# Kernel tuning notes

Hardware: AMD Instinct MI355X
Metric: run time of the kernel (lower is better)

## Reference

```python
import jax, jax.numpy as jnp
import numpy as np

N_NODES = 100000

def gcn_conv(x, W, b, src, dst):
    n = x.shape[0]
    loop = jnp.arange(n, dtype=src.dtype)
    src_f = jnp.concatenate([src, loop])
    dst_f = jnp.concatenate([dst, loop])
    deg = jax.ops.segment_sum(jnp.ones_like(src_f, dtype=x.dtype), dst_f, num_segments=n)
    dinv = jnp.where(deg > 0, deg ** -0.5, 0.0)
    norm = dinv[src_f] * dinv[dst_f]              # [E+N]
    h = x @ W                                      # [N, out]
    msg = h[src_f] * norm[:, None]                 # gather + scale
    out = jax.ops.segment_sum(msg, dst_f, num_segments=n)
    return out + b

def setup_inputs() -> dict:
    key = jax.random.key(0)
    k1, k2, k3, k4, k5 = jax.random.split(key, 5)
    d = 128
    x = jax.random.normal(k1, (N_NODES, d), dtype=jnp.float32)
    e = jax.random.randint(k2, (2, 3200000), 0, N_NODES, dtype=jnp.int64)
    # Glorot-style init as in PyG GCNConv
    W1 = jax.random.normal(k3, (d, 64), dtype=jnp.float32) * (1.0 / np.sqrt(d))
    b1 = jnp.zeros((64,), dtype=jnp.float32)
    W2 = jax.random.normal(k4, (64, 1), dtype=jnp.float32) * (1.0 / np.sqrt(64))
    b2 = jnp.zeros((1,), dtype=jnp.float32)
    return {"x": x, "e": e, "W1": W1, "b1": b1, "W2": W2, "b2": b2}

def reference(x, e, W1, b1, W2, b2):
    src, dst = e[0], e[1]
    h = jax.nn.relu(gcn_conv(x, W1, b1, src, dst))
    return gcn_conv(h, W2, b2, src, dst)
```

## Files before the change

### kernel.cpp

```cpp
#include <hip/hip_runtime.h>
#include <hip/hip_bf16.h>


typedef short s8_t __attribute__((ext_vector_type(8)));
typedef float f4_t __attribute__((ext_vector_type(4)));

__device__ __forceinline__ float bf2f(unsigned short u) {
    union { unsigned int u; float f; } c; c.u = ((unsigned int)u) << 16; return c.f;
}
__device__ __forceinline__ unsigned short f2bf(float f) {
    union { float f; unsigned int u; } c; c.f = f;
    unsigned int u = c.u;
    unsigned int r = (u + 0x7fffu + ((u >> 16) & 1u)) >> 16;
    return (unsigned short)r;
}
__device__ __forceinline__ float loadF(const void* p, int i, int isbf) {
    return isbf ? bf2f(((const unsigned short*)p)[i]) : ((const float*)p)[i];
}
__device__ __forceinline__ int edgeIdx(const void* e, long long i, int is64) {
    return is64 ? (int)((const long long*)e)[i] : ((const int*)e)[i];
}

__global__ void k_detect(const void* e, const void* x, int* flags) {
    int lane = threadIdx.x;
    unsigned int ew = ((const unsigned int*)e)[2 * lane + 1];
    unsigned long long nz = __ballot(ew != 0);
    unsigned int xw = ((const unsigned int*)x)[lane];
    unsigned int low = xw & 0xffffu;
    unsigned int e8 = (low >> 7) & 0xffu;
    bool plaus = (low == 0u) || (e8 >= 110u && e8 <= 135u);
    unsigned long long pl = __ballot(plaus);
    if (lane == 0) {
        flags[0] = (nz == 0ull) ? 1 : 0;
        flags[1] = (__popcll(pl) > 32) ? 1 : 0;
    }
}

__global__ void k_prep(const void* W1, unsigned short* __restrict__ wT,
                       const int* flags) {
    if (!flags[1]) return;
    int tid = threadIdx.x;
    const unsigned short* w = (const unsigned short*)W1;
    for (int idx = tid; idx < 128 * 64; idx += 256) {
        int k = idx >> 6, n = idx & 63;
        wT[n * 128 + k] = w[idx];
    }
}

__global__ void k_prep32(const void* W1, unsigned short* __restrict__ wTh,
                         unsigned short* __restrict__ wTl, const int* flags) {
    if (flags[1]) return;
    int tid = threadIdx.x;
    const float* w = (const float*)W1;
    for (int idx = tid; idx < 128 * 64; idx += 256) {
        int k = idx >> 6, n = idx & 63;
        float v = w[idx];
        unsigned short h = f2bf(v);
        wTh[n * 128 + k] = h;
        wTl[n * 128 + k] = f2bf(v - bf2f(h));
    }
}

__launch_bounds__(256)
__global__ void k_hist(const void* e, int* __restrict__ histT, const int* flags,
                       int E, int B, int HB) {
    __shared__ int hist[1024];
    int tid = threadIdx.x;
    int is64 = flags[0];
    for (int f = tid; f < B; f += 256) hist[f] = 0;
    __syncthreads();
    int base = blockIdx.x * 4096;
    #pragma unroll
    for (int k = 0; k < 16; ++k) {
        int i = base + k * 256 + tid;
        if (i < E) {
            int d = edgeIdx(e, (long long)E + i, is64);
            atomicAdd(&hist[d >> 9], 1);
        }
    }
    __syncthreads();
    for (int f = tid; f < B; f += 256)
        histT[(long long)f * HB + blockIdx.x] = hist[f];
}

__global__ void k_scanA(int* __restrict__ data, int* __restrict__ partial, int M) {
    __shared__ int s[256];
    int tid = threadIdx.x;
    int i = blockIdx.x * 256 + tid;
    int v = (i < M) ? data[i] : 0;
    s[tid] = v; __syncthreads();
    for (int off = 1; off < 256; off <<= 1) {
        int t = (tid >= off) ? s[tid - off] : 0;
        __syncthreads(); s[tid] += t; __syncthreads();
    }
    if (i < M) data[i] = s[tid] - v;
    if (tid == 255) partial[blockIdx.x] = s[255];
}

__global__ void k_scanB(int* __restrict__ partial, int nP) {
    __shared__ int s[1024];
    int tid = threadIdx.x;
    int C = (nP + 1023) >> 10;
    int base = tid * C;
    int v[8]; int tot = 0;
    for (int j = 0; j < C; ++j) { v[j] = (base + j < nP) ? partial[base + j] : 0; tot += v[j]; }
    s[tid] = tot; __syncthreads();
    for (int off = 1; off < 1024; off <<= 1) {
        int t = (tid >= off) ? s[tid - off] : 0;
        __syncthreads(); s[tid] += t; __syncthreads();
    }
    int run = s[tid] - tot;
    for (int j = 0; j < C; ++j) { if (base + j < nP) { int tmp = v[j]; partial[base + j] = run; run += tmp; } }
}

__global__ void k_scanC(int* __restrict__ data, const int* __restrict__ partial,
                        int* __restrict__ bucketStart, int M, int HB, int B, int E) {
    int f = blockIdx.x * 256 + threadIdx.x;
    if (f < M) {
        int val = data[f] + partial[f >> 8];
        data[f] = val;
        int q = f / HB;
        if (f - q * HB == 0) bucketStart[q] = val;
    }
    if (f == 0) bucketStart[B] = E;
}

__launch_bounds__(256)
__global__ void k_part(const void* e, const int* __restrict__ histT,
                       int* __restrict__ part, const int* flags,
                       int E, int B, int HB) {
    __shared__ int lcur[1024];
    int tid = threadIdx.x;
    int is64 = flags[0];
    for (int f = tid; f < B; f += 256)
        lcur[f] = histT[(long long)f * HB + blockIdx.x];
    __syncthreads();
    int base = blockIdx.x * 4096;
    #pragma unroll
    for (int k = 0; k < 16; ++k) {
        int i = base + k * 256 + tid;
        if (i < E) {
            int s = edgeIdx(e, i, is64);
            int d = edgeIdx(e, (long long)E + i, is64);
            int pos = atomicAdd(&lcur[d >> 9], 1);
            part[pos] = s | ((d & 511) << 17);
        }
    }
}

__launch_bounds__(512)
__global__ void k_sort2(const int* __restrict__ part, const int* __restrict__ bucketStart,
                        int* __restrict__ srcSorted, int* __restrict__ start,
                        float* __restrict__ dinv, int N, int B) {
    __shared__ int cnt[512];
    __shared__ int s[512];
    __shared__ int cur[512];
    int tid = threadIdx.x, b = blockIdx.x;
    cnt[tid] = 0;
    __syncthreads();
    int lo = bucketStart[b], hi = bucketStart[b + 1];
    for (int idx = lo + tid; idx < hi; idx += 512)
        atomicAdd(&cnt[(part[idx] >> 17) & 511], 1);
    __syncthreads();
    int v = cnt[tid];
    s[tid] = v; __syncthreads();
    for (int off = 1; off < 512; off <<= 1) {
        int t = (tid >= off) ? s[tid - off] : 0;
        __syncthreads(); s[tid] += t; __syncthreads();
    }
    int base_ = lo + s[tid] - v;
    cur[tid] = base_;
    int node = b * 512 + tid;
    if (node < N) {
        start[node] = base_;
        dinv[node] = rsqrtf((float)(v + 1));
    }
    if (b == 0 && tid == 0) start[N] = bucketStart[B];
    __syncthreads();
    for (int idx = lo + tid; idx < hi; idx += 512) {
        int pw = part[idx];
        int pos = atomicAdd(&cur[(pw >> 17) & 511], 1);
        srcSorted[pos] = pw & 0x1FFFF;
    }
}

__launch_bounds__(256)
__global__ void k_gemm_bf(const void* x, const unsigned short* __restrict__ wT,
                          const float* __restrict__ dinv,
                          unsigned short* __restrict__ hb, const int* flags, int N) {
    if (!flags[1]) return;
    int tid = threadIdx.x;
    int lane = tid & 63, wv = tid >> 6;
    int q = lane >> 4, r = lane & 15;
    const unsigned short* xb = (const unsigned short*)x;
    int gw = blockIdx.x * 4 + wv;
    int nW = gridDim.x * 4;
    int RB = (N + 15) >> 4;
    for (int rb = gw; rb < RB; rb += nW) {
        int row0 = rb * 16;
        int arow = row0 + r;
        s8_t a[4];
        #pragma unroll
        for (int kk = 0; kk < 4; ++kk)
            a[kk] = (arow < N)
                ? *(const s8_t*)&xb[(long long)arow * 128 + kk * 32 + q * 8]
                : (s8_t)(short)0;
        f4_t acc[4];
        #pragma unroll
        for (int nt = 0; nt < 4; ++nt) acc[nt] = (f4_t){0.f, 0.f, 0.f, 0.f};
        #pragma unroll
        for (int nt = 0; nt < 4; ++nt) {
            #pragma unroll
            for (int kk = 0; kk < 4; ++kk) {
                s8_t b = *(const s8_t*)&wT[(nt * 16 + r) * 128 + kk * 32 + q * 8];
                acc[nt] = __builtin_amdgcn_mfma_f32_16x16x32_bf16(a[kk], b, acc[nt], 0, 0, 0);
            }
        }
        #pragma unroll
        for (int reg = 0; reg < 4; ++reg) {
            int row = row0 + q * 4 + reg;
            if (row < N) {
                float dv = dinv[row];
                #pragma unroll
                for (int nt = 0; nt < 4; ++nt)
                    hb[(long long)row * 64 + nt * 16 + r] = f2bf(acc[nt][reg] * dv);
            }
        }
    }
}

__launch_bounds__(256)
__global__ void k_gemm_x32(const void* x, const unsigned short* __restrict__ wTh,
                           const unsigned short* __restrict__ wTl,
                           const float* __restrict__ dinv,
                           unsigned short* __restrict__ hb, const int* flags, int N) {
    if (flags[1]) return;
    int tid = threadIdx.x;
    int lane = tid & 63, wv = tid >> 6;
    int q = lane >> 4, r = lane & 15;
    const float* xf = (const float*)x;
    int gw = blockIdx.x * 4 + wv;
    int nW = gridDim.x * 4;
    int RB = (N + 15) >> 4;
    for (int rb = gw; rb < RB; rb += nW) {
        int row0 = rb * 16;
        int arow = row0 + r;
        s8_t ah[4], al[4];
        #pragma unroll
        for (int kk = 0; kk < 4; ++kk) {
            f4_t x0 = (f4_t){0.f, 0.f, 0.f, 0.f}, x1 = x0;
            if (arow < N) {
                const float* p = &xf[(long long)arow * 128 + kk * 32 + q * 8];
                x0 = *(const f4_t*)p;
                x1 = *(const f4_t*)(p + 4);
            }
            #pragma unroll
            for (int j = 0; j < 4; ++j) {
                unsigned short h0 = f2bf(x0[j]);
                ah[kk][j] = (short)h0;
                al[kk][j] = (short)f2bf(x0[j] - bf2f(h0));
                unsigned short h1 = f2bf(x1[j]);
                ah[kk][4 + j] = (short)h1;
                al[kk][4 + j] = (short)f2bf(x1[j] - bf2f(h1));
            }
        }
        f4_t acc[4];
        #pragma unroll
        for (int nt = 0; nt < 4; ++nt) acc[nt] = (f4_t){0.f, 0.f, 0.f, 0.f};
        #pragma unroll
        for (int nt = 0; nt < 4; ++nt) {
            #pragma unroll
            for (int kk = 0; kk < 4; ++kk) {
                s8_t bh = *(const s8_t*)&wTh[(nt * 16 + r) * 128 + kk * 32 + q * 8];
                s8_t bl = *(const s8_t*)&wTl[(nt * 16 + r) * 128 + kk * 32 + q * 8];
                acc[nt] = __builtin_amdgcn_mfma_f32_16x16x32_bf16(ah[kk], bh, acc[nt], 0, 0, 0);
                acc[nt] = __builtin_amdgcn_mfma_f32_16x16x32_bf16(al[kk], bh, acc[nt], 0, 0, 0);
                acc[nt] = __builtin_amdgcn_mfma_f32_16x16x32_bf16(ah[kk], bl, acc[nt], 0, 0, 0);
            }
        }
        #pragma unroll
        for (int reg = 0; reg < 4; ++reg) {
            int row = row0 + q * 4 + reg;
            if (row < N) {
                float dv = dinv[row];
                #pragma unroll
                for (int nt = 0; nt < 4; ++nt)
                    hb[(long long)row * 64 + nt * 16 + r] = f2bf(acc[nt][reg] * dv);
            }
        }
    }
}

__launch_bounds__(256)
__global__ void k_agg1(const unsigned short* __restrict__ hb,
                       const float* __restrict__ dinv,
                       const int* __restrict__ start,
                       const int* __restrict__ srcSorted,
                       const void* b1, const void* W2, float* __restrict__ sbuf2,
                       const int* flags, int N) {
    int lane = threadIdx.x & 63;
    int node = (blockIdx.x * blockDim.x + threadIdx.x) >> 6;
    if (node >= N) return;
    int isbf = flags[1];
    float di = dinv[node];
    int base = start[node], cnt = start[node + 1] - base;
    float acc = bf2f(hb[(long long)node * 64 + lane]);
    for (int c = 0; c < cnt; c += 64) {
        int t = c + lane;
        int sidx = (t < cnt) ? srcSorted[base + t] : 0;
        int m = cnt - c; if (m > 64) m = 64;
        int t2 = 0;
        for (; t2 + 16 <= m; t2 += 16) {
            int s0  = __shfl(sidx, t2 + 0),  s1  = __shfl(sidx, t2 + 1);
            int s2  = __shfl(sidx, t2 + 2),  s3  = __shfl(sidx, t2 + 3);
            int s4  = __shfl(sidx, t2 + 4),  s5  = __shfl(sidx, t2 + 5);
            int s6  = __shfl(sidx, t2 + 6),  s7  = __shfl(sidx, t2 + 7);
            int s8  = __shfl(sidx, t2 + 8),  s9  = __shfl(sidx, t2 + 9);
            int s10 = __shfl(sidx, t2 + 10), s11 = __shfl(sidx, t2 + 11);
            int s12 = __shfl(sidx, t2 + 12), s13 = __shfl(sidx, t2 + 13);
            int s14 = __shfl(sidx, t2 + 14), s15 = __shfl(sidx, t2 + 15);
            unsigned short v0  = hb[(long long)s0  * 64 + lane];
            unsigned short v1  = hb[(long long)s1  * 64 + lane];
            unsigned short v2  = hb[(long long)s2  * 64 + lane];
            unsigned short v3  = hb[(long long)s3  * 64 + lane];
            unsigned short v4  = hb[(long long)s4  * 64 + lane];
            unsigned short v5  = hb[(long long)s5  * 64 + lane];
            unsigned short v6  = hb[(long long)s6  * 64 + lane];
            unsigned short v7  = hb[(long long)s7  * 64 + lane];
            unsigned short v8  = hb[(long long)s8  * 64 + lane];
            unsigned short v9  = hb[(long long)s9  * 64 + lane];
            unsigned short v10 = hb[(long long)s10 * 64 + lane];
            unsigned short v11 = hb[(long long)s11 * 64 + lane];
            unsigned short v12 = hb[(long long)s12 * 64 + lane];
            unsigned short v13 = hb[(long long)s13 * 64 + lane];
            unsigned short v14 = hb[(long long)s14 * 64 + lane];
            unsigned short v15 = hb[(long long)s15 * 64 + lane];
            acc += bf2f(v0);  acc += bf2f(v1);  acc += bf2f(v2);  acc += bf2f(v3);
            acc += bf2f(v4);  acc += bf2f(v5);  acc += bf2f(v6);  acc += bf2f(v7);
            acc += bf2f(v8);  acc += bf2f(v9);  acc += bf2f(v10); acc += bf2f(v11);
            acc += bf2f(v12); acc += bf2f(v13); acc += bf2f(v14); acc += bf2f(v15);
        }
        for (; t2 + 8 <= m; t2 += 8) {
            int s0 = __shfl(sidx, t2 + 0), s1 = __shfl(sidx, t2 + 1);
            int s2 = __shfl(sidx, t2 + 2), s3 = __shfl(sidx, t2 + 3);
            int s4 = __shfl(sidx, t2 + 4), s5 = __shfl(sidx, t2 + 5);
            int s6 = __shfl(sidx, t2 + 6), s7 = __shfl(sidx, t2 + 7);
            unsigned short v0 = hb[(long long)s0 * 64 + lane];
            unsigned short v1 = hb[(long long)s1 * 64 + lane];
            unsigned short v2 = hb[(long long)s2 * 64 + lane];
            unsigned short v3 = hb[(long long)s3 * 64 + lane];
            unsigned short v4 = hb[(long long)s4 * 64 + lane];
            unsigned short v5 = hb[(long long)s5 * 64 + lane];
            unsigned short v6 = hb[(long long)s6 * 64 + lane];
            unsigned short v7 = hb[(long long)s7 * 64 + lane];
            acc += bf2f(v0); acc += bf2f(v1); acc += bf2f(v2); acc += bf2f(v3);
            acc += bf2f(v4); acc += bf2f(v5); acc += bf2f(v6); acc += bf2f(v7);
        }
        for (; t2 < m; ++t2) {
            int s0 = __shfl(sidx, t2);
            acc += bf2f(hb[(long long)s0 * 64 + lane]);
        }
    }
    float v = acc * di + loadF(b1, lane, isbf);
    v = fmaxf(v, 0.f);
    float p = v * loadF(W2, lane, isbf);
    #pragma unroll
    for (int o = 32; o >= 1; o >>= 1) p += __shfl_xor(p, o);
    if (lane == 0) sbuf2[node] = p * di;
}

__launch_bounds__(256)
__global__ void k_agg2(const float* __restrict__ sbuf2, const float* __restrict__ dinv,
                       const int* __restrict__ start,
                       const int* __restrict__ srcSorted,
                       const void* b2, void* out, const int* flags, int N) {
    int lane = threadIdx.x & 63;
    int node = (blockIdx.x * blockDim.x + threadIdx.x) >> 6;
    if (node >= N) return;
    int isbf = flags[1];
    float di = dinv[node];
    int base = start[node], cnt = start[node + 1] - base;
    float part = 0.f;
    for (int t = lane; t < cnt; t += 64) part += sbuf2[srcSorted[base + t]];
    #pragma unroll
    for (int o = 32; o >= 1; o >>= 1) part += __shfl_xor(part, o);
    if (lane == 0) {
        float o_ = (part + sbuf2[node]) * di + loadF(b2, 0, isbf);
        if (isbf) ((unsigned short*)out)[node] = f2bf(o_);
        else      ((float*)out)[node] = o_;
    }
}

extern "C" void kernel_launch(void* const* d_in, const int* in_sizes, int n_in,
                              void* d_out, int out_size, void* d_ws, size_t ws_size,
                              hipStream_t stream) {
    const void* x  = d_in[0];
    const void* e  = d_in[1];
    const void* W1 = d_in[2];
    const void* b1 = d_in[3];
    const void* W2 = d_in[4];
    const void* b2 = d_in[5];
    int N = in_sizes[0] / 128;
    int E = in_sizes[1] / 2;
    int B  = (N + 511) / 512;
    int HB = (E + 4095) / 4096;
    int M  = B * HB;
    int nP = (M + 255) / 256;
    int NB = B * 512;
    int EP = ((E + 255) / 256) * 256;
    int RB = (N + 15) / 16;
    int GG = (RB + 3) / 4;

    int*   wsI         = (int*)d_ws;
    int*   flags       = wsI;
    unsigned short* wT  = (unsigned short*)(wsI + 256);
    unsigned short* wTh = (unsigned short*)(wsI + 256 + 4096);
    unsigned short* wTl = (unsigned short*)(wsI + 256 + 8192);
    int*   histT       = wsI + 256 + 12288;
    int*   partial     = histT + ((M + 255) / 256) * 256;
    int*   bucketStart = partial + ((nP + 255) / 256) * 256;
    float* dinv        = (float*)(bucketStart + 1040);
    float* sbuf2       = dinv + NB;
    int*   start       = (int*)(sbuf2 + NB);
    int*   srcSorted   = start + NB + 256;
    int*   part        = srcSorted + EP;
    unsigned short* hb = (unsigned short*)part;

    hipLaunchKernelGGL(k_detect, dim3(1), dim3(64), 0, stream, e, x, flags);
    hipLaunchKernelGGL(k_prep, dim3(1), dim3(256), 0, stream, W1, wT, flags);
    hipLaunchKernelGGL(k_prep32, dim3(1), dim3(256), 0, stream, W1, wTh, wTl, flags);
    hipLaunchKernelGGL(k_hist, dim3(HB), dim3(256), 0, stream, e, histT, flags, E, B, HB);
    hipLaunchKernelGGL(k_scanA, dim3(nP), dim3(256), 0, stream, histT, partial, M);
    hipLaunchKernelGGL(k_scanB, dim3(1), dim3(1024), 0, stream, partial, nP);
    hipLaunchKernelGGL(k_scanC, dim3(nP), dim3(256), 0, stream,
                       histT, partial, bucketStart, M, HB, B, E);
    hipLaunchKernelGGL(k_part, dim3(HB), dim3(256), 0, stream, e, histT, part, flags, E, B, HB);
    hipLaunchKernelGGL(k_sort2, dim3(B), dim3(512), 0, stream,
                       part, bucketStart, srcSorted, start, dinv, N, B);
    hipLaunchKernelGGL(k_gemm_bf, dim3(GG), dim3(256), 0, stream,
                       x, wT, dinv, hb, flags, N);
    hipLaunchKernelGGL(k_gemm_x32, dim3(GG), dim3(256), 0, stream,
                       x, wTh, wTl, dinv, hb, flags, N);
    hipLaunchKernelGGL(k_agg1, dim3((N + 3) / 4), dim3(256), 0, stream,
                       hb, dinv, start, srcSorted, b1, W2, sbuf2, flags, N);
    hipLaunchKernelGGL(k_agg2, dim3((N + 3) / 4), dim3(256), 0, stream,
                       sbuf2, dinv, start, srcSorted, b2, d_out, flags, N);
}
```

Before: 332.0 us.

## Split hidden features into quarter tables and aggregate 16 nodes per wave

The GEMM output is stored as four column-quarter tables of 16 bf16 features each, instead of one 64-wide row-major table. The first aggregation now has each wave handle 16 nodes and sweep the four quarter tables, with each 16-lane group gathering a different edge. The intent is to shrink the working set per gather pass so each quarter table fits better in cache, and to make gathered accesses 32-byte segments. It also merges the two prep kernels and the two GEMM kernels into single launches, and replaces round-to-nearest with truncation when splitting fp32 into hi/lo bf16. The cost is reading the edge lists four times and more complex control flow, and truncation slightly changes rounding.

```diff
diff --git a/kernel.cpp b/kernel.cpp
--- a/kernel.cpp
+++ b/kernel.cpp
@@ -4,6 +4,8 @@
 
 typedef short s8_t __attribute__((ext_vector_type(8)));
 typedef float f4_t __attribute__((ext_vector_type(4)));
+
+#define NPW 16
 
 __device__ __forceinline__ float bf2f(unsigned short u) {
     union { unsigned int u; float f; } c; c.u = ((unsigned int)u) << 16; return c.f;
@@ -36,28 +38,25 @@
     }
 }
 
-__global__ void k_prep(const void* W1, unsigned short* __restrict__ wT,
-                       const int* flags) {
-    if (!flags[1]) return;
-    int tid = threadIdx.x;
-    const unsigned short* w = (const unsigned short*)W1;
-    for (int idx = tid; idx < 128 * 64; idx += 256) {
-        int k = idx >> 6, n = idx & 63;
-        wT[n * 128 + k] = w[idx];
-    }
-}
-
-__global__ void k_prep32(const void* W1, unsigned short* __restrict__ wTh,
-                         unsigned short* __restrict__ wTl, const int* flags) {
-    if (flags[1]) return;
-    int tid = threadIdx.x;
-    const float* w = (const float*)W1;
-    for (int idx = tid; idx < 128 * 64; idx += 256) {
-        int k = idx >> 6, n = idx & 63;
-        float v = w[idx];
-        unsigned short h = f2bf(v);
-        wTh[n * 128 + k] = h;
-        wTl[n * 128 + k] = f2bf(v - bf2f(h));
+__global__ void k_prep_all(const void* W1, unsigned short* __restrict__ wT,
+                           unsigned short* __restrict__ wTh,
+                           unsigned short* __restrict__ wTl, const int* flags) {
+    int tid = threadIdx.x;
+    if (flags[1]) {
+        const unsigned short* w = (const unsigned short*)W1;
+        for (int idx = tid; idx < 128 * 64; idx += 256) {
+            int k = idx >> 6, n = idx & 63;
+            wT[n * 128 + k] = w[idx];
+        }
+    } else {
+        const float* w = (const float*)W1;
+        for (int idx = tid; idx < 128 * 64; idx += 256) {
+            int k = idx >> 6, n = idx & 63;
+            float v = w[idx];
+            unsigned short h = f2bf(v);
+            wTh[n * 128 + k] = h;
+            wTl[n * 128 + k] = f2bf(v - bf2f(h));
+        }
     }
 }
 
@@ -185,35 +184,76 @@
 }
 
 __launch_bounds__(256)
-__global__ void k_gemm_bf(const void* x, const unsigned short* __restrict__ wT,
-                          const float* __restrict__ dinv,
-                          unsigned short* __restrict__ hb, const int* flags, int N) {
-    if (!flags[1]) return;
+__global__ void k_gemm(const void* x, const unsigned short* __restrict__ wT,
+                       const unsigned short* __restrict__ wTh,
+                       const unsigned short* __restrict__ wTl,
+                       const float* __restrict__ dinv,
+                       unsigned short* __restrict__ hbq, const int* flags, int N) {
     int tid = threadIdx.x;
     int lane = tid & 63, wv = tid >> 6;
     int q = lane >> 4, r = lane & 15;
-    const unsigned short* xb = (const unsigned short*)x;
     int gw = blockIdx.x * 4 + wv;
     int nW = gridDim.x * 4;
     int RB = (N + 15) >> 4;
+    int isbf = flags[1];
     for (int rb = gw; rb < RB; rb += nW) {
         int row0 = rb * 16;
         int arow = row0 + r;
-        s8_t a[4];
-        #pragma unroll
-        for (int kk = 0; kk < 4; ++kk)
-            a[kk] = (arow < N)
-                ? *(const s8_t*)&xb[(long long)arow * 128 + kk * 32 + q * 8]
-                : (s8_t)(short)0;
         f4_t acc[4];
         #pragma unroll
         for (int nt = 0; nt < 4; ++nt) acc[nt] = (f4_t){0.f, 0.f, 0.f, 0.f};
-        #pragma unroll
-        for (int nt = 0; nt < 4; ++nt) {
+        if (isbf) {
+            const unsigned short* xb = (const unsigned short*)x;
+            s8_t a[4];
+            #pragma unroll
+            for (int kk = 0; kk < 4; ++kk)
+                a[kk] = (arow < N)
+                    ? *(const s8_t*)&xb[(long long)arow * 128 + kk * 32 + q * 8]
+                    : (s8_t)(short)0;
+            #pragma unroll
+            for (int nt = 0; nt < 4; ++nt) {
+                #pragma unroll
+                for (int kk = 0; kk < 4; ++kk) {
+                    s8_t b = *(const s8_t*)&wT[(nt * 16 + r) * 128 + kk * 32 + q * 8];
+                    acc[nt] = __builtin_amdgcn_mfma_f32_16x16x32_bf16(a[kk], b, acc[nt], 0, 0, 0);
+                }
+            }
+        } else {
+            const float* xf = (const float*)x;
+            s8_t ah[4], al[4];
             #pragma unroll
             for (int kk = 0; kk < 4; ++kk) {
-                s8_t b = *(const s8_t*)&wT[(nt * 16 + r) * 128 + kk * 32 + q * 8];
-                acc[nt] = __builtin_amdgcn_mfma_f32_16x16x32_bf16(a[kk], b, acc[nt], 0, 0, 0);
+                f4_t x0 = (f4_t){0.f, 0.f, 0.f, 0.f}, x1 = x0;
+                if (arow < N) {
+                    const float* p = &xf[(long long)arow * 128 + kk * 32 + q * 8];
+                    x0 = *(const f4_t*)p;
+                    x1 = *(const f4_t*)(p + 4);
+                }
+                #pragma unroll
+                for (int j = 0; j < 4; ++j) {
+                    union { float f; unsigned int u; } c0, h0, r0, c1, h1, r1;
+                    c0.f = x0[j];
+                    h0.u = c0.u & 0xffff0000u;
+                    ah[kk][j] = (short)(c0.u >> 16);
+                    r0.f = x0[j] - h0.f;
+                    al[kk][j] = (short)(r0.u >> 16);
+                    c1.f = x1[j];
+                    h1.u = c1.u & 0xffff0000u;
+                    ah[kk][4 + j] = (short)(c1.u >> 16);
+                    r1.f = x1[j] - h1.f;
+                    al[kk][4 + j] = (short)(r1.u >> 16);
+                }
+            }
+            #pragma unroll
+            for (int nt = 0; nt < 4; ++nt) {
+                #pragma unroll
+                for (int kk = 0; kk < 4; ++kk) {
+                    s8_t bh = *(const s8_t*)&wTh[(nt * 16 + r) * 128 + kk * 32 + q * 8];
+                    s8_t bl = *(const s8_t*)&wTl[(nt * 16 + r) * 128 + kk * 32 + q * 8];
+                    acc[nt] = __builtin_amdgcn_mfma_f32_16x16x32_bf16(ah[kk], bh, acc[nt], 0, 0, 0);
+                    acc[nt] = __builtin_amdgcn_mfma_f32_16x16x32_bf16(al[kk], bh, acc[nt], 0, 0, 0);
+                    acc[nt] = __builtin_amdgcn_mfma_f32_16x16x32_bf16(ah[kk], bl, acc[nt], 0, 0, 0);
+                }
             }
         }
         #pragma unroll
@@ -223,150 +263,82 @@
                 float dv = dinv[row];
                 #pragma unroll
                 for (int nt = 0; nt < 4; ++nt)
-                    hb[(long long)row * 64 + nt * 16 + r] = f2bf(acc[nt][reg] * dv);
+                    hbq[((long long)nt * N + row) * 16 + r] = f2bf(acc[nt][reg] * dv);
             }
         }
     }
 }
 
 __launch_bounds__(256)
-__global__ void k_gemm_x32(const void* x, const unsigned short* __restrict__ wTh,
-                           const unsigned short* __restrict__ wTl,
-                           const float* __restrict__ dinv,
-                           unsigned short* __restrict__ hb, const int* flags, int N) {
-    if (flags[1]) return;
-    int tid = threadIdx.x;
-    int lane = tid & 63, wv = tid >> 6;
-    int q = lane >> 4, r = lane & 15;
-    const float* xf = (const float*)x;
-    int gw = blockIdx.x * 4 + wv;
-    int nW = gridDim.x * 4;
-    int RB = (N + 15) >> 4;
-    for (int rb = gw; rb < RB; rb += nW) {
-        int row0 = rb * 16;
-        int arow = row0 + r;
-        s8_t ah[4], al[4];
-        #pragma unroll
-        for (int kk = 0; kk < 4; ++kk) {
-            f4_t x0 = (f4_t){0.f, 0.f, 0.f, 0.f}, x1 = x0;
-            if (arow < N) {
-                const float* p = &xf[(long long)arow * 128 + kk * 32 + q * 8];
-                x0 = *(const f4_t*)p;
-                x1 = *(const f4_t*)(p + 4);
-            }
-            #pragma unroll
-            for (int j = 0; j < 4; ++j) {
-                unsigned short h0 = f2bf(x0[j]);
-                ah[kk][j] = (short)h0;
-                al[kk][j] = (short)f2bf(x0[j] - bf2f(h0));
-                unsigned short h1 = f2bf(x1[j]);
-                ah[kk][4 + j] = (short)h1;
-                al[kk][4 + j] = (short)f2bf(x1[j] - bf2f(h1));
-            }
-        }
-        f4_t acc[4];
-        #pragma unroll
-        for (int nt = 0; nt < 4; ++nt) acc[nt] = (f4_t){0.f, 0.f, 0.f, 0.f};
-        #pragma unroll
-        for (int nt = 0; nt < 4; ++nt) {
-            #pragma unroll
-            for (int kk = 0; kk < 4; ++kk) {
-                s8_t bh = *(const s8_t*)&wTh[(nt * 16 + r) * 128 + kk * 32 + q * 8];
-                s8_t bl = *(const s8_t*)&wTl[(nt * 16 + r) * 128 + kk * 32 + q * 8];
-                acc[nt] = __builtin_amdgcn_mfma_f32_16x16x32_bf16(ah[kk], bh, acc[nt], 0, 0, 0);
-                acc[nt] = __builtin_amdgcn_mfma_f32_16x16x32_bf16(al[kk], bh, acc[nt], 0, 0, 0);
-                acc[nt] = __builtin_amdgcn_mfma_f32_16x16x32_bf16(ah[kk], bl, acc[nt], 0, 0, 0);
-            }
-        }
-        #pragma unroll
-        for (int reg = 0; reg < 4; ++reg) {
-            int row = row0 + q * 4 + reg;
-            if (row < N) {
-                float dv = dinv[row];
-                #pragma unroll
-                for (int nt = 0; nt < 4; ++nt)
-                    hb[(long long)row * 64 + nt * 16 + r] = f2bf(acc[nt][reg] * dv);
-            }
-        }
-    }
-}
-
-__launch_bounds__(256)
-__global__ void k_agg1(const unsigned short* __restrict__ hb,
+__global__ void k_agg1(const unsigned short* __restrict__ hbq,
                        const float* __restrict__ dinv,
                        const int* __restrict__ start,
                        const int* __restrict__ srcSorted,
                        const void* b1, const void* W2, float* __restrict__ sbuf2,
                        const int* flags, int N) {
     int lane = threadIdx.x & 63;
-    int node = (blockIdx.x * blockDim.x + threadIdx.x) >> 6;
-    if (node >= N) return;
+    int wid = (blockIdx.x * blockDim.x + threadIdx.x) >> 6;
+    int g = lane >> 4, r = lane & 15;
+    int n0 = wid * NPW;
+    if (n0 >= N) return;
+    float acc[NPW];
+    #pragma unroll
+    for (int i = 0; i < NPW; ++i) acc[i] = 0.f;
+    for (int q = 0; q < 4; ++q) {
+        const unsigned short* tab = hbq + (long long)q * N * 16;
+        #pragma unroll
+        for (int i = 0; i < NPW; ++i) {
+            int node = n0 + i;
+            if (node < N) {
+                int base = start[node];
+                int cnt  = start[node + 1] - base;
+                float a = 0.f;
+                for (int c = 0; c < cnt; c += 64) {
+                    int t = c + lane;
+                    int sidx = (t < cnt) ? srcSorted[base + t] : 0;
+                    int m = cnt - c; if (m > 64) m = 64;
+                    int t2 = 0;
+                    for (; t2 + 16 <= m; t2 += 16) {
+                        int e0 = __shfl(sidx, t2 + g);
+                        int e1 = __shfl(sidx, t2 + 4 + g);
+                        int e2 = __shfl(sidx, t2 + 8 + g);
+                        int e3 = __shfl(sidx, t2 + 12 + g);
+                        unsigned short v0 = tab[e0 * 16 + r];
+                        unsigned short v1 = tab[e1 * 16 + r];
+                        unsigned short v2 = tab[e2 * 16 + r];
+                        unsigned short v3 = tab[e3 * 16 + r];
+                        a += bf2f(v0); a += bf2f(v1);
+                        a += bf2f(v2); a += bf2f(v3);
+                    }
+                    for (; t2 < m; t2 += 4) {
+                        int e0 = __shfl(sidx, t2 + g);
+                        unsigned short v0 = tab[e0 * 16 + r];
+                        a += (t2 + g < m) ? bf2f(v0) : 0.f;
+                    }
+                }
+                a += __shfl_xor(a, 16);
+                a += __shfl_xor(a, 32);
+                acc[i] = (g == q) ? a : acc[i];
+            }
+        }
+    }
     int isbf = flags[1];
-    float di = dinv[node];
-    int base = start[node], cnt = start[node + 1] - base;
-    float acc = bf2f(hb[(long long)node * 64 + lane]);
-    for (int c = 0; c < cnt; c += 64) {
-        int t = c + lane;
-        int sidx = (t < cnt) ? srcSorted[base + t] : 0;
-        int m = cnt - c; if (m > 64) m = 64;
-        int t2 = 0;
-        for (; t2 + 16 <= m; t2 += 16) {
-            int s0  = __shfl(sidx, t2 + 0),  s1  = __shfl(sidx, t2 + 1);
-            int s2  = __shfl(sidx, t2 + 2),  s3  = __shfl(sidx, t2 + 3);
-            int s4  = __shfl(sidx, t2 + 4),  s5  = __shfl(sidx, t2 + 5);
-            int s6  = __shfl(sidx, t2 + 6),  s7  = __shfl(sidx, t2 + 7);
-            int s8  = __shfl(sidx, t2 + 8),  s9  = __shfl(sidx, t2 + 9);
-            int s10 = __shfl(sidx, t2 + 10), s11 = __shfl(sidx, t2 + 11);
-            int s12 = __shfl(sidx, t2 + 12), s13 = __shfl(sidx, t2 + 13);
-            int s14 = __shfl(sidx, t2 + 14), s15 = __shfl(sidx, t2 + 15);
-            unsigned short v0  = hb[(long long)s0  * 64 + lane];
-            unsigned short v1  = hb[(long long)s1  * 64 + lane];
-            unsigned short v2  = hb[(long long)s2  * 64 + lane];
-            unsigned short v3  = hb[(long long)s3  * 64 + lane];
-            unsigned short v4  = hb[(long long)s4  * 64 + lane];
-            unsigned short v5  = hb[(long long)s5  * 64 + lane];
-            unsigned short v6  = hb[(long long)s6  * 64 + lane];
-            unsigned short v7  = hb[(long long)s7  * 64 + lane];
-            unsigned short v8  = hb[(long long)s8  * 64 + lane];
-            unsigned short v9  = hb[(long long)s9  * 64 + lane];
-            unsigned short v10 = hb[(long long)s10 * 64 + lane];
-            unsigned short v11 = hb[(long long)s11 * 64 + lane];
-            unsigned short v12 = hb[(long long)s12 * 64 + lane];
-            unsigned short v13 = hb[(long long)s13 * 64 + lane];
-            unsigned short v14 = hb[(long long)s14 * 64 + lane];
-            unsigned short v15 = hb[(long long)s15 * 64 + lane];
-            acc += bf2f(v0);  acc += bf2f(v1);  acc += bf2f(v2);  acc += bf2f(v3);
-            acc += bf2f(v4);  acc += bf2f(v5);  acc += bf2f(v6);  acc += bf2f(v7);
-            acc += bf2f(v8);  acc += bf2f(v9);  acc += bf2f(v10); acc += bf2f(v11);
-            acc += bf2f(v12); acc += bf2f(v13); acc += bf2f(v14); acc += bf2f(v15);
-        }
-        for (; t2 + 8 <= m; t2 += 8) {
-            int s0 = __shfl(sidx, t2 + 0), s1 = __shfl(sidx, t2 + 1);
-            int s2 = __shfl(sidx, t2 + 2), s3 = __shfl(sidx, t2 + 3);
-            int s4 = __shfl(sidx, t2 + 4), s5 = __shfl(sidx, t2 + 5);
-            int s6 = __shfl(sidx, t2 + 6), s7 = __shfl(sidx, t2 + 7);
-            unsigned short v0 = hb[(long long)s0 * 64 + lane];
-            unsigned short v1 = hb[(long long)s1 * 64 + lane];
-            unsigned short v2 = hb[(long long)s2 * 64 + lane];
-            unsigned short v3 = hb[(long long)s3 * 64 + lane];
-            unsigned short v4 = hb[(long long)s4 * 64 + lane];
-            unsigned short v5 = hb[(long long)s5 * 64 + lane];
-            unsigned short v6 = hb[(long long)s6 * 64 + lane];
-            unsigned short v7 = hb[(long long)s7 * 64 + lane];
-            acc += bf2f(v0); acc += bf2f(v1); acc += bf2f(v2); acc += bf2f(v3);
-            acc += bf2f(v4); acc += bf2f(v5); acc += bf2f(v6); acc += bf2f(v7);
-        }
-        for (; t2 < m; ++t2) {
-            int s0 = __shfl(sidx, t2);
-            acc += bf2f(hb[(long long)s0 * 64 + lane]);
-        }
-    }
-    float v = acc * di + loadF(b1, lane, isbf);
-    v = fmaxf(v, 0.f);
-    float p = v * loadF(W2, lane, isbf);
+    float b1v = loadF(b1, lane, isbf);
+    float w2v = loadF(W2, lane, isbf);
     #pragma unroll
-    for (int o = 32; o >= 1; o >>= 1) p += __shfl_xor(p, o);
-    if (lane == 0) sbuf2[node] = p * di;
+    for (int i = 0; i < NPW; ++i) {
+        int node = n0 + i;
+        if (node < N) {
+            float di = dinv[node];
+            unsigned short sv = hbq[((long long)g * N + node) * 16 + r];
+            float v = (acc[i] + bf2f(sv)) * di + b1v;
+            v = fmaxf(v, 0.f);
+            float p = v * w2v;
+            #pragma unroll
+            for (int o = 32; o >= 1; o >>= 1) p += __shfl_xor(p, o);
+            if (lane == 0) sbuf2[node] = p * di;
+        }
+    }
 }
 
 __launch_bounds__(256)
@@ -410,6 +382,7 @@
     int EP = ((E + 255) / 256) * 256;
     int RB = (N + 15) / 16;
     int GG = (RB + 3) / 4;
+    int AW = (RB + 3) / 4;
 
     int*   wsI         = (int*)d_ws;
     int*   flags       = wsI;
@@ -424,11 +397,10 @@
     int*   start       = (int*)(sbuf2 + NB);
     int*   srcSorted   = start + NB + 256;
     int*   part        = srcSorted + EP;
-    unsigned short* hb = (unsigned short*)part;
+    unsigned short* hbq = (unsigned short*)part;
 
     hipLaunchKernelGGL(k_detect, dim3(1), dim3(64), 0, stream, e, x, flags);
-    hipLaunchKernelGGL(k_prep, dim3(1), dim3(256), 0, stream, W1, wT, flags);
-    hipLaunchKernelGGL(k_prep32, dim3(1), dim3(256), 0, stream, W1, wTh, wTl, flags);
+    hipLaunchKernelGGL(k_prep_all, dim3(1), dim3(256), 0, stream, W1, wT, wTh, wTl, flags);
     hipLaunchKernelGGL(k_hist, dim3(HB), dim3(256), 0, stream, e, histT, flags, E, B, HB);
     hipLaunchKernelGGL(k_scanA, dim3(nP), dim3(256), 0, stream, histT, partial, M);
     hipLaunchKernelGGL(k_scanB, dim3(1), dim3(1024), 0, stream, partial, nP);
@@ -437,12 +409,10 @@
     hipLaunchKernelGGL(k_part, dim3(HB), dim3(256), 0, stream, e, histT, part, flags, E, B, HB);
     hipLaunchKernelGGL(k_sort2, dim3(B), dim3(512), 0, stream,
                        part, bucketStart, srcSorted, start, dinv, N, B);
-    hipLaunchKernelGGL(k_gemm_bf, dim3(GG), dim3(256), 0, stream,
-                       x, wT, dinv, hb, flags, N);
-    hipLaunchKernelGGL(k_gemm_x32, dim3(GG), dim3(256), 0, stream,
-                       x, wTh, wTl, dinv, hb, flags, N);
-    hipLaunchKernelGGL(k_agg1, dim3((N + 3) / 4), dim3(256), 0, stream,
-                       hb, dinv, start, srcSorted, b1, W2, sbuf2, flags, N);
+    hipLaunchKernelGGL(k_gemm, dim3(GG), dim3(256), 0, stream,
+                       x, wT, wTh, wTl, dinv, hbq, flags, N);
+    hipLaunchKernelGGL(k_agg1, dim3(AW), dim3(256), 0, stream,
+                       hbq, dinv, start, srcSorted, b1, W2, sbuf2, flags, N);
     hipLaunchKernelGGL(k_agg2, dim3((N + 3) / 4), dim3(256), 0, stream,
                        sbuf2, dinv, start, srcSorted, b2, d_out, flags, N);
 }
```

After: 401.3 us. 20.9% more time.
